# Optimization experiments

Measured on AMD Instinct MI355X. Metric: run time of the kernel, lower is better.

Reference implementation:

```python
import jax, jax.numpy as jnp
import numpy as np

N = 50000      # nodes
E = 800000     # edges (avg degree 16)
NF = 128       # input feature dim
H = 128        # hidden dim
GAMMA = 1.0    # gm init arg
COS_EPS = 1e-8 # F.cosine_similarity eps
EW_MIN = 1e-4  # edge-weight clamp


def setup_inputs() -> dict:
    key = jax.random.key(0)
    ks = jax.random.split(key, 9)
    x = jax.random.normal(ks[0], (N, NF), dtype=jnp.float32)
    edge_index = jax.random.randint(ks[1], (2, E), 0, N, dtype=jnp.int64)
    sensitive_attr = jax.random.randint(ks[2], (N,), 0, 2, dtype=jnp.int64)
    s1 = 1.0 / np.sqrt(NF)
    s2 = 1.0 / np.sqrt(H)
    W1 = jax.random.normal(ks[3], (NF, H), dtype=jnp.float32) * s1
    b1 = jnp.zeros((H,), dtype=jnp.float32)
    W2 = jax.random.normal(ks[4], (H, H), dtype=jnp.float32) * s2
    b2 = jnp.zeros((H,), dtype=jnp.float32)
    Wc = jax.random.normal(ks[5], (H, 1), dtype=jnp.float32) * s2
    bc = jnp.zeros((1,), dtype=jnp.float32)
    return {"x": x, "edge_index": edge_index, "sensitive_attr": sensitive_attr,
            "W1": W1, "b1": b1, "W2": W2, "b2": b2, "Wc": Wc, "bc": bc}


def gcn_conv(x, W, b, src, dst, ew, n):
    """PyG GCNConv: lin -> symmetric-normalized edge-weighted aggregation (+self loops) -> bias."""
    xt = x @ W                                              # [N,H]
    deg = jax.ops.segment_sum(ew, dst, num_segments=n) + 1.0  # self-loop weight 1
    dinv = jnp.where(deg > 0, deg ** -0.5, 0.0)             # [N]
    norm = dinv[src] * ew * dinv[dst]                       # [E]
    agg = jax.ops.segment_sum(xt[src] * norm[:, None], dst, num_segments=n)
    # self-loop contribution: norm_ii = dinv[i] * 1 * dinv[i]
    return agg + xt * (dinv * dinv)[:, None] + b


def reference(x, edge_index, sensitive_attr, W1, b1, W2, b2, Wc, bc):
    src, dst = edge_index[0], edge_index[1]
    # cosine-similarity edge weights (gather-heavy)
    xs, xd = x[src], x[dst]                                  # [E,F] each
    dot = jnp.sum(xs * xd, axis=1)
    ns = jnp.maximum(jnp.sqrt(jnp.sum(xs * xs, axis=1)), COS_EPS)
    nd = jnp.maximum(jnp.sqrt(jnp.sum(xd * xd, axis=1)), COS_EPS)
    sim = dot / (ns * nd)
    sen_diff = (sensitive_attr[src] != sensitive_attr[dst]).astype(x.dtype)
    ew = jnp.maximum(sim * jnp.exp(-GAMMA * sen_diff), EW_MIN)
    # two GCN layers (dropout is identity in eval mode)
    h = jax.nn.relu(gcn_conv(x, W1, b1, src, dst, ew, N))
    h = jax.nn.relu(gcn_conv(h, W2, b2, src, dst, ew, N))
    y = h @ Wc + bc                                          # [N,1]
    return (y, h)
```

## Files before the change

kernel.cpp:

```cpp
#include <hip/hip_runtime.h>


typedef unsigned short u16;
typedef unsigned int u32;
typedef __attribute__((ext_vector_type(8))) short short8;
typedef __attribute__((ext_vector_type(4))) float floatx4;

__device__ __forceinline__ float bflo(u32 u){ return __uint_as_float(u << 16); }
__device__ __forceinline__ float bfhi(u32 u){ return __uint_as_float(u & 0xFFFF0000u); }
__device__ __forceinline__ float bf1(u16 u){ return __uint_as_float(((u32)u) << 16); }
__device__ __forceinline__ u16 f2bf(float f){
    u32 u = __float_as_uint(f);
    u += 0x7FFFu + ((u >> 16) & 1u);
    return (u16)(u >> 16);
}
__device__ __forceinline__ u32 pack2(float a, float b){
    return (u32)f2bf(a) | ((u32)f2bf(b) << 16);
}
__device__ __forceinline__ float wsum(float v){
#pragma unroll
    for (int o = 32; o > 0; o >>= 1) v += __shfl_xor(v, o, 64);
    return v;
}
__device__ __forceinline__ float ld1(const void* p, size_t idx, int f32){
    return f32 ? ((const float*)p)[idx] : bf1(((const u16*)p)[idx]);
}
__device__ __forceinline__ int ldidx(const int* p, size_t i, int i64){
    return i64 ? p[2 * i] : p[i];
}

__global__ void classify_k(const u32* __restrict__ xw, const int* __restrict__ eiw,
                           int* __restrict__ flags)
{
    __shared__ int c_out, c_nz;
    int t = threadIdx.x;
    if (t == 0) { c_out = 0; c_nz = 0; }
    __syncthreads();
    u32 w = xw[t];
    int e = (w >> 7) & 0xFF;
    int outl = (e < 110 || e > 140) ? 1 : 0;
    int nz = (eiw[2 * t + 1] != 0) ? 1 : 0;
    atomicAdd(&c_out, outl);
    atomicAdd(&c_nz, nz);
    __syncthreads();
    if (t == 0) { flags[0] = (c_out > 256); flags[1] = (c_nz < 256); }
}

__global__ __launch_bounds__(256) void convhist_k(const void* __restrict__ x,
                                                  u32* __restrict__ xb,
                                                  float* __restrict__ rn, int N,
                                                  const int* __restrict__ ei,
                                                  const int* __restrict__ sa,
                                                  int* __restrict__ cnt, int E,
                                                  const void* __restrict__ W1,
                                                  const void* __restrict__ W2,
                                                  uint4* __restrict__ wf1,
                                                  uint4* __restrict__ wf2,
                                                  const int* __restrict__ flags,
                                                  int nbN, int nbE)
{
    int b = blockIdx.x;
    if (b < nbN) {
        int i = b * 4 + (threadIdx.x >> 6);
        if (i >= N) return;
        int lane = threadIdx.x & 63;
        u32 u;
        if (flags[0]) {
            const float* q = (const float*)x + (size_t)i * 128 + lane * 2;
            u = pack2(q[0], q[1]);
        } else u = ((const u32*)x)[(size_t)i * 64 + lane];
        xb[(size_t)i * 64 + lane] = u;
        float f0 = bflo(u), f1 = bfhi(u);
        float ss = wsum(f0 * f0 + f1 * f1);
        if (lane == 0) {
            float r = 1.0f / fmaxf(sqrtf(ss), 1e-8f);
            int a = flags[1] ? sa[2 * (size_t)i] : sa[i];
            rn[i] = a ? -r : r;
        }
    } else if (b < nbN + nbE) {
        int e = (b - nbN) * 256 + threadIdx.x;
        if (e >= E) return;
        int d = ldidx(ei, (size_t)E + e, flags[1]);
        if ((u32)d >= (u32)N) d = 0;
        atomicAdd(&cnt[d], 1);
    } else {
        int slot = (b - nbN - nbE) * 256 + threadIdx.x;
        if (slot >= 4096) return;
        int f32w = flags[0];
        const void* W = (slot < 2048) ? W1 : W2;
        uint4* wf = (slot < 2048) ? wf1 : wf2;
        int s = slot & 2047;
        int lane = s & 63, kk = (s >> 6) & 3, ct = s >> 8;
        int q = lane >> 4, n = lane & 15;
        int col = ct * 16 + n, k0 = kk * 32 + q * 8;
        union { u16 us[8]; uint4 u4; } tmp;
#pragma unroll
        for (int j = 0; j < 8; ++j)
            tmp.us[j] = f2bf(ld1(W, (size_t)(k0 + j) * 128 + col, f32w));
        wf[s] = tmp.u4;
    }
}

__global__ __launch_bounds__(256) void scanA_k(int* __restrict__ cnt,
                                               int* __restrict__ rowp,
                                               int* __restrict__ bsum, int N)
{
    __shared__ int wtot[4];
    int t = threadIdx.x, lane = t & 63, w = t >> 6;
    int i0 = blockIdx.x * 1024 + t * 4;
    int v[4];
#pragma unroll
    for (int k = 0; k < 4; ++k) {
        int i = i0 + k;
        v[k] = (i < N) ? cnt[i] : 0;
        if (i < N) cnt[i] = 0;
    }
    int t4 = v[0] + v[1] + v[2] + v[3];
    int sc = t4;
#pragma unroll
    for (int o = 1; o < 64; o <<= 1) {
        int nv = __shfl_up(sc, o);
        if (lane >= o) sc += nv;
    }
    if (lane == 63) wtot[w] = sc;
    __syncthreads();
    int wo = 0, tot = 0;
#pragma unroll
    for (int k = 0; k < 4; ++k) { int s = wtot[k]; if (k < w) wo += s; tot += s; }
    int pre = wo + sc - t4;
#pragma unroll
    for (int k = 0; k < 4; ++k) {
        int i = i0 + k;
        if (i < N) rowp[i] = pre;
        pre += v[k];
    }
    if (t == 0) bsum[blockIdx.x] = tot;
}

__global__ void scanB_k(int* __restrict__ bsum, int* __restrict__ rowp,
                        int nb, int N)
{
    int lane = threadIdx.x;
    int carry = 0;
    for (int base = 0; base < nb; base += 64) {
        int i = base + lane;
        int v = (i < nb) ? bsum[i] : 0;
        int sc = v;
#pragma unroll
        for (int o = 1; o < 64; o <<= 1) {
            int nv = __shfl_up(sc, o);
            if (lane >= o) sc += nv;
        }
        if (i < nb) bsum[i] = carry + sc - v;
        carry += __shfl(sc, 63);
    }
    if (lane == 0) rowp[N] = carry;
}

__global__ __launch_bounds__(256) void scanC_k(int* __restrict__ rowp,
                                               const int* __restrict__ bsum, int N)
{
    int off = bsum[blockIdx.x];
    int i0 = blockIdx.x * 1024 + threadIdx.x * 4;
#pragma unroll
    for (int k = 0; k < 4; ++k) {
        int i = i0 + k;
        if (i < N) rowp[i] += off;
    }
}

__global__ __launch_bounds__(256) void scat_k(const int* __restrict__ ei,
                                              const int* __restrict__ rowp,
                                              int* __restrict__ cnt,
                                              u32* __restrict__ rec,
                                              int E, int N,
                                              const int* __restrict__ flags)
{
    int e = blockIdx.x * 256 + threadIdx.x;
    if (e >= E) return;
    int i64 = flags[1];
    int s = ldidx(ei, e, i64);
    int d = ldidx(ei, (size_t)E + e, i64);
    if ((u32)s >= (u32)N) s = 0;
    if ((u32)d >= (u32)N) d = 0;
    int pos = rowp[d] + atomicAdd(&cnt[d], 1);
    if ((u32)pos >= (u32)E) pos = 0;
    rec[pos] = (u32)s;
}

__global__ __launch_bounds__(256) void ewcsr_k(const u32* __restrict__ xb,
                                               const float* __restrict__ rn,
                                               const int* __restrict__ rowp,
                                               u32* __restrict__ rec,
                                               float* __restrict__ dv,
                                               int N, int E)
{
    int i = blockIdx.x * 4 + (threadIdx.x >> 6);
    if (i >= N) return;
    int lane = threadIdx.x & 63, g = lane >> 4, j = lane & 15;
    uint4 D = ((const uint4*)(xb + (size_t)i * 64))[j];
    float rni = rn[i];
    int p0 = rowp[i], p1 = rowp[i + 1];
    if (p0 < 0) p0 = 0;
    if (p1 > E) p1 = E;
    float acc = 0.0f;
    int p = p0 + g;
    for (; p + 4 < p1; p += 8) {
        int s0 = (int)rec[p];     if ((u32)s0 >= (u32)N) s0 = 0;
        int s1 = (int)rec[p + 4]; if ((u32)s1 >= (u32)N) s1 = 0;
        uint4 A0 = ((const uint4*)(xb + (size_t)s0 * 64))[j];
        uint4 A1 = ((const uint4*)(xb + (size_t)s1 * 64))[j];
        float d0 = bflo(A0.x) * bflo(D.x) + bfhi(A0.x) * bfhi(D.x)
                 + bflo(A0.y) * bflo(D.y) + bfhi(A0.y) * bfhi(D.y)
                 + bflo(A0.z) * bflo(D.z) + bfhi(A0.z) * bfhi(D.z)
                 + bflo(A0.w) * bflo(D.w) + bfhi(A0.w) * bfhi(D.w);
        float d1 = bflo(A1.x) * bflo(D.x) + bfhi(A1.x) * bfhi(D.x)
                 + bflo(A1.y) * bflo(D.y) + bfhi(A1.y) * bfhi(D.y)
                 + bflo(A1.z) * bflo(D.z) + bfhi(A1.z) * bfhi(D.z)
                 + bflo(A1.w) * bflo(D.w) + bfhi(A1.w) * bfhi(D.w);
#pragma unroll
        for (int o = 8; o > 0; o >>= 1) {
            d0 += __shfl_xor(d0, o);
            d1 += __shfl_xor(d1, o);
        }
        if (j == 0) {
            float pr0 = rn[s0] * rni;
            float w0 = fmaxf(d0 * fabsf(pr0) *
                             ((pr0 < 0.0f) ? 0.36787944117144233f : 1.0f), 1e-4f);
            u16 wb0 = f2bf(w0);
            rec[p] = ((u32)s0 << 16) | wb0;
            acc += bf1(wb0);
            float pr1 = rn[s1] * rni;
            float w1 = fmaxf(d1 * fabsf(pr1) *
                             ((pr1 < 0.0f) ? 0.36787944117144233f : 1.0f), 1e-4f);
            u16 wb1 = f2bf(w1);
            rec[p + 4] = ((u32)s1 << 16) | wb1;
            acc += bf1(wb1);
        }
    }
    if (p < p1) {
        int s0 = (int)rec[p]; if ((u32)s0 >= (u32)N) s0 = 0;
        uint4 A0 = ((const uint4*)(xb + (size_t)s0 * 64))[j];
        float d0 = bflo(A0.x) * bflo(D.x) + bfhi(A0.x) * bfhi(D.x)
                 + bflo(A0.y) * bflo(D.y) + bfhi(A0.y) * bfhi(D.y)
                 + bflo(A0.z) * bflo(D.z) + bfhi(A0.z) * bfhi(D.z)
                 + bflo(A0.w) * bflo(D.w) + bfhi(A0.w) * bfhi(D.w);
#pragma unroll
        for (int o = 8; o > 0; o >>= 1) d0 += __shfl_xor(d0, o);
        if (j == 0) {
            float pr0 = rn[s0] * rni;
            float w0 = fmaxf(d0 * fabsf(pr0) *
                             ((pr0 < 0.0f) ? 0.36787944117144233f : 1.0f), 1e-4f);
            u16 wb0 = f2bf(w0);
            rec[p] = ((u32)s0 << 16) | wb0;
            acc += bf1(wb0);
        }
    }
    acc += __shfl_xor(acc, 16);
    acc += __shfl_xor(acc, 32);
    if (lane == 0) dv[i] = 1.0f / sqrtf(1.0f + acc);
}

__global__ __launch_bounds__(256) void agg_k(const u32* __restrict__ feat,
                                             const int* __restrict__ rowp,
                                             const u32* __restrict__ rec,
                                             const float* __restrict__ dinv,
                                             u32* __restrict__ Tb, int N, int E)
{
    int i = blockIdx.x * 4 + (threadIdx.x >> 6);
    if (i >= N) return;
    int lane = threadIdx.x & 63;
    float di = dinv[i], sc = di * di;
    u32 u = feat[(size_t)i * 64 + lane];
    float a0 = bflo(u) * sc, a1 = bfhi(u) * sc;
    int p0 = rowp[i], p1 = rowp[i + 1];
    if (p0 < 0) p0 = 0;
    if (p1 > E) p1 = E;
    int p = p0;
    for (; p + 7 < p1; p += 8) {
        u32 r[8]; int s[8]; u32 v[8];
#pragma unroll
        for (int k = 0; k < 8; ++k) {
            r[k] = rec[p + k];
            s[k] = r[k] >> 16;
            if (s[k] >= N) s[k] = 0;
        }
#pragma unroll
        for (int k = 0; k < 8; ++k) v[k] = feat[(size_t)s[k] * 64 + lane];
#pragma unroll
        for (int k = 0; k < 8; ++k) {
            float w = bf1((u16)r[k]) * di * dinv[s[k]];
            a0 = fmaf(w, bflo(v[k]), a0);
            a1 = fmaf(w, bfhi(v[k]), a1);
        }
    }
    for (; p + 1 < p1; p += 2) {
        u32 r0 = rec[p], r1 = rec[p + 1];
        int s0 = r0 >> 16, s1 = r1 >> 16;
        if (s0 >= N) s0 = 0;
        if (s1 >= N) s1 = 0;
        u32 v0 = feat[(size_t)s0 * 64 + lane];
        u32 v1 = feat[(size_t)s1 * 64 + lane];
        float w0 = bf1((u16)r0) * di * dinv[s0];
        float w1 = bf1((u16)r1) * di * dinv[s1];
        a0 = fmaf(w0, bflo(v0), a0); a1 = fmaf(w0, bfhi(v0), a1);
        a0 = fmaf(w1, bflo(v1), a0); a1 = fmaf(w1, bfhi(v1), a1);
    }
    if (p < p1) {
        u32 r0 = rec[p];
        int s0 = r0 >> 16;
        if (s0 >= N) s0 = 0;
        u32 v0 = feat[(size_t)s0 * 64 + lane];
        float w0 = bf1((u16)r0) * di * dinv[s0];
        a0 = fmaf(w0, bflo(v0), a0); a1 = fmaf(w0, bfhi(v0), a1);
    }
    Tb[(size_t)i * 64 + lane] = pack2(a0, a1);
}

__global__ __launch_bounds__(256) void gemm_m(const u32* __restrict__ Tb,
                                              const uint4* __restrict__ wfrag,
                                              const void* __restrict__ bias,
                                              void* __restrict__ out, int outbf,
                                              int N,
                                              const void* __restrict__ Wc,
                                              const void* __restrict__ bc,
                                              float* __restrict__ yout,
                                              const int* __restrict__ flags)
{
    int t = threadIdx.x, wave = t >> 6, lane = t & 63;
    int q = lane >> 4, n = lane & 15;
    int f32w = flags[0];
    int rowbase = blockIdx.x * 64 + wave * 16;
    int arow = rowbase + n; if (arow > N - 1) arow = N - 1;
    const uint4* ap = (const uint4*)(Tb + (size_t)arow * 64);
    short8 a[4];
#pragma unroll
    for (int kk = 0; kk < 4; ++kk) {
        uint4 av = ap[kk * 4 + q];
        a[kk] = *(short8*)&av;
    }
    floatx4 acc[8];
#pragma unroll
    for (int ct = 0; ct < 8; ++ct) acc[ct] = (floatx4){0.f, 0.f, 0.f, 0.f};
#pragma unroll
    for (int ct = 0; ct < 8; ++ct) {
#pragma unroll
        for (int kk = 0; kk < 4; ++kk) {
            uint4 bv = wfrag[(ct * 4 + kk) * 64 + lane];
            acc[ct] = __builtin_amdgcn_mfma_f32_16x16x32_bf16(
                a[kk], *(short8*)&bv, acc[ct], 0, 0, 0);
        }
    }
    float bcv = 0.0f;
    float part[4] = {0.f, 0.f, 0.f, 0.f};
    if (yout) bcv = ld1(bc, 0, f32w);
#pragma unroll
    for (int ct = 0; ct < 8; ++ct) {
        int col = ct * 16 + n;
        float bia = ld1(bias, col, f32w);
        float wcv = yout ? ld1(Wc, col, f32w) : 0.0f;
#pragma unroll
        for (int r = 0; r < 4; ++r) {
            int row = rowbase + q * 4 + r;
            float h = fmaxf(acc[ct][r] + bia, 0.0f);
            if (row < N) {
                if (outbf) ((u16*)out)[(size_t)row * 128 + col] = f2bf(h);
                else       ((float*)out)[(size_t)row * 128 + col] = h;
            }
            part[r] = fmaf(h, wcv, part[r]);
        }
    }
    if (yout) {
#pragma unroll
        for (int r = 0; r < 4; ++r) {
            float pr = part[r];
#pragma unroll
            for (int o = 8; o > 0; o >>= 1) pr += __shfl_xor(pr, o);
            int row = rowbase + q * 4 + r;
            if (n == 0 && row < N) yout[row] = pr + bcv;
        }
    }
}

extern "C" void kernel_launch(void* const* d_in, const int* in_sizes, int n_in,
                              void* d_out, int out_size, void* d_ws, size_t ws_size,
                              hipStream_t stream)
{
    const void* x  = d_in[0];
    const int* ei  = (const int*)d_in[1];
    const int* sa  = (const int*)d_in[2];
    const void* W1 = d_in[3];
    const void* b1 = d_in[4];
    const void* W2 = d_in[5];
    const void* b2 = d_in[6];
    const void* Wc = d_in[7];
    const void* bc = d_in[8];
    const int N = in_sizes[2];
    const int E = in_sizes[1] / 2;

    float* y_out = (float*)d_out;
    float* h_out = y_out + N;
    u32*   Tbuf  = (u32*)d_in[0];

    const int nbN = (N + 3) / 4, nbE = (E + 255) / 256;
    const int nbS = (N + 1023) / 1024;

    char* p = (char*)d_ws;
    auto carve = [&](size_t bytes) { char* r = p; p += (bytes + 255) & ~(size_t)255; return r; };
    int*   flags = (int*)carve(256);
    float* rn    = (float*)carve((size_t)N * 4);
    float* dinv  = (float*)carve((size_t)N * 4);
    int*   cnt   = (int*)carve((size_t)N * 4);
    int*   rowp  = (int*)carve((size_t)(N + 1) * 4);
    int*   bsum  = (int*)carve((size_t)nbS * 4);
    uint4* wf1   = (uint4*)carve(2048 * 16);
    uint4* wf2   = (uint4*)carve(2048 * 16);
    u32*   rec   = (u32*)carve((size_t)E * 4);
    u32*   xb    = (u32*)carve((size_t)N * 64 * 4);

    classify_k<<<1, 1024, 0, stream>>>((const u32*)x, ei, flags);
    hipMemsetAsync(cnt, 0, (size_t)N * 4, stream);
    convhist_k<<<nbN + nbE + 16, 256, 0, stream>>>(x, xb, rn, N, ei, sa, cnt, E,
                                                   W1, W2, wf1, wf2, flags,
                                                   nbN, nbE);
    scanA_k<<<nbS, 256, 0, stream>>>(cnt, rowp, bsum, N);
    scanB_k<<<1, 64, 0, stream>>>(bsum, rowp, nbS, N);
    scanC_k<<<nbS, 256, 0, stream>>>(rowp, bsum, N);
    scat_k<<<(E + 255) / 256, 256, 0, stream>>>(ei, rowp, cnt, rec, E, N, flags);
    ewcsr_k<<<(N + 3) / 4, 256, 0, stream>>>(xb, rn, rowp, rec, dinv, N, E);

    agg_k<<<(N + 3) / 4, 256, 0, stream>>>(xb, rowp, rec, dinv, Tbuf, N, E);
    gemm_m<<<(N + 63) / 64, 256, 0, stream>>>(Tbuf, wf1, b1, xb, 1, N,
                                              nullptr, nullptr, nullptr, flags);
    agg_k<<<(N + 3) / 4, 256, 0, stream>>>(xb, rowp, rec, dinv, Tbuf, N, E);
    gemm_m<<<(N + 63) / 64, 256, 0, stream>>>(Tbuf, wf2, b2, h_out, 0, N,
                                              Wc, bc, y_out, flags);
}
```

Baseline: 329.5 us.

## Replace direct CSR scatter with two-pass coarse bucketing by destination block

The single-pass scatter that placed each edge into CSR order with global atomics is replaced by two passes. First, edges are partitioned into 256-node destination buckets using shared-memory histograms and one global atomic per bucket per block, and written to a temp buffer. Then one block per bucket scatters its edges into the final CSR slots, so the per-node atomics and writes stay within a small region. The aim is better locality for the random atomics and writes, at the cost of an extra read/write pass and an extra launch. The x input buffer is reused as temp storage. With 50000 nodes there are about 196 buckets, within the 256-entry bcur array, but larger N would overflow it.

```diff
diff --git a/kernel.cpp b/kernel.cpp
--- a/kernel.cpp
+++ b/kernel.cpp
@@ -158,34 +158,85 @@
 }
 
 __global__ __launch_bounds__(256) void scanC_k(int* __restrict__ rowp,
-                                               const int* __restrict__ bsum, int N)
+                                               const int* __restrict__ bsum,
+                                               int* __restrict__ bcur, int N)
 {
     int off = bsum[blockIdx.x];
     int i0 = blockIdx.x * 1024 + threadIdx.x * 4;
 #pragma unroll
     for (int k = 0; k < 4; ++k) {
         int i = i0 + k;
-        if (i < N) rowp[i] += off;
-    }
-}
-
-__global__ __launch_bounds__(256) void scat_k(const int* __restrict__ ei,
-                                              const int* __restrict__ rowp,
-                                              int* __restrict__ cnt,
-                                              u32* __restrict__ rec,
-                                              int E, int N,
-                                              const int* __restrict__ flags)
-{
-    int e = blockIdx.x * 256 + threadIdx.x;
-    if (e >= E) return;
+        if (i < N) {
+            int v = rowp[i] + off;
+            rowp[i] = v;
+            if ((i & 255) == 0) bcur[i >> 8] = v;
+        }
+    }
+}
+
+__global__ __launch_bounds__(256) void bucket_k(const int* __restrict__ ei,
+                                                int* __restrict__ bcur,
+                                                u32* __restrict__ tmp,
+                                                int E, int N,
+                                                const int* __restrict__ flags)
+{
+    __shared__ int lh[256];
+    __shared__ int gb[256];
+    int t = threadIdx.x;
+    lh[t] = 0;
+    __syncthreads();
     int i64 = flags[1];
-    int s = ldidx(ei, e, i64);
-    int d = ldidx(ei, (size_t)E + e, i64);
-    if ((u32)s >= (u32)N) s = 0;
-    if ((u32)d >= (u32)N) d = 0;
-    int pos = rowp[d] + atomicAdd(&cnt[d], 1);
-    if ((u32)pos >= (u32)E) pos = 0;
-    rec[pos] = (u32)s;
+    size_t base = (size_t)blockIdx.x * 4096;
+    u32 pay[16], meta[16];
+#pragma unroll
+    for (int k = 0; k < 16; ++k) {
+        size_t e = base + (size_t)k * 256 + t;
+        if (e < (size_t)E) {
+            int s = ldidx(ei, e, i64);
+            int d = ldidx(ei, (size_t)E + e, i64);
+            if ((u32)s >= (u32)N) s = 0;
+            if ((u32)d >= (u32)N) d = 0;
+            int b = d >> 8;
+            pay[k] = ((u32)s << 8) | ((u32)d & 0xFFu);
+            int r = atomicAdd(&lh[b], 1);
+            meta[k] = ((u32)r << 8) | (u32)b;
+        } else meta[k] = 0xFFFFFFFFu;
+    }
+    __syncthreads();
+    int c = lh[t];
+    gb[t] = c ? atomicAdd(&bcur[t], c) : 0;
+    __syncthreads();
+#pragma unroll
+    for (int k = 0; k < 16; ++k) {
+        if (meta[k] != 0xFFFFFFFFu) {
+            int b = (int)(meta[k] & 0xFFu);
+            int r = (int)(meta[k] >> 8);
+            tmp[gb[b] + r] = pay[k];
+        }
+    }
+}
+
+__global__ __launch_bounds__(256) void scat2_k(const int* __restrict__ rowp,
+                                               int* __restrict__ cnt,
+                                               const u32* __restrict__ tmp,
+                                               u32* __restrict__ rec,
+                                               int N, int E)
+{
+    int b = blockIdx.x, t = threadIdx.x;
+    int n0 = b << 8;
+    int n1 = n0 + 256; if (n1 > N) n1 = N;
+    int p0 = rowp[n0], p1 = rowp[n1];
+    if (p0 < 0) p0 = 0;
+    if (p1 > E) p1 = E;
+    for (int idx = p0 + t; idx < p1; idx += 256) {
+        u32 pay = tmp[idx];
+        int d = n0 | (int)(pay & 0xFFu);
+        if (d >= N) d = N - 1;
+        int s = (int)(pay >> 8);
+        int pos = rowp[d] + atomicAdd(&cnt[d], 1);
+        if ((u32)pos >= (u32)E) pos = 0;
+        rec[pos] = (u32)s;
+    }
 }
 
 __global__ __launch_bounds__(256) void ewcsr_k(const u32* __restrict__ xb,
@@ -401,9 +452,11 @@
     float* y_out = (float*)d_out;
     float* h_out = y_out + N;
     u32*   Tbuf  = (u32*)d_in[0];
+    u32*   tmp   = (u32*)d_in[0];
 
     const int nbN = (N + 3) / 4, nbE = (E + 255) / 256;
     const int nbS = (N + 1023) / 1024;
+    const int NB  = (N + 255) / 256;
 
     char* p = (char*)d_ws;
     auto carve = [&](size_t bytes) { char* r = p; p += (bytes + 255) & ~(size_t)255; return r; };
@@ -413,6 +466,7 @@
     int*   cnt   = (int*)carve((size_t)N * 4);
     int*   rowp  = (int*)carve((size_t)(N + 1) * 4);
     int*   bsum  = (int*)carve((size_t)nbS * 4);
+    int*   bcur  = (int*)carve(256 * 4);
     uint4* wf1   = (uint4*)carve(2048 * 16);
     uint4* wf2   = (uint4*)carve(2048 * 16);
     u32*   rec   = (u32*)carve((size_t)E * 4);
@@ -425,8 +479,9 @@
                                                    nbN, nbE);
     scanA_k<<<nbS, 256, 0, stream>>>(cnt, rowp, bsum, N);
     scanB_k<<<1, 64, 0, stream>>>(bsum, rowp, nbS, N);
-    scanC_k<<<nbS, 256, 0, stream>>>(rowp, bsum, N);
-    scat_k<<<(E + 255) / 256, 256, 0, stream>>>(ei, rowp, cnt, rec, E, N, flags);
+    scanC_k<<<nbS, 256, 0, stream>>>(rowp, bsum, bcur, N);
+    bucket_k<<<(E + 4095) / 4096, 256, 0, stream>>>(ei, bcur, tmp, E, N, flags);
+    scat2_k<<<NB, 256, 0, stream>>>(rowp, cnt, tmp, rec, N, E);
     ewcsr_k<<<(N + 3) / 4, 256, 0, stream>>>(xb, rn, rowp, rec, dinv, N, E);
 
     agg_k<<<(N + 3) / 4, 256, 0, stream>>>(xb, rowp, rec, dinv, Tbuf, N, E);
```

New measurement: 317.3 us. 1.04x faster.
